# Kernel tuning notes

Measured on AMD Instinct MI355X. Metric: run time of the kernel, lower is better.

The kernel has to match this reference:

```python
import jax, jax.numpy as jnp
import numpy as np

HEADS = 16
KEY_SIZE = 64
SIZE_PER_HEAD = 64
OUT_DIM = HEADS * SIZE_PER_HEAD  # 1024
BIG = 1e10
B, LQ, LK = 2, 2048, 2048


def setup_inputs() -> dict:
    key = jax.random.key(0)
    ks = jax.random.split(key, 8)
    q = jax.random.normal(ks[0], (B, LQ, OUT_DIM), dtype=jnp.float32)
    k = jax.random.normal(ks[1], (B, LK, OUT_DIM), dtype=jnp.float32)
    v = jax.random.normal(ks[2], (B, LK, OUT_DIM), dtype=jnp.float32)
    v_mask = (jax.random.uniform(ks[3], (B, LK)) > 0.1).astype(jnp.float32)
    q_mask = (jax.random.uniform(ks[4], (B, LQ)) > 0.1).astype(jnp.float32)
    # bias-free Linear weights, torch layout [out_features, in_features]
    s = 1.0 / np.sqrt(OUT_DIM)
    Wq = jax.random.normal(ks[5], (HEADS * KEY_SIZE, OUT_DIM), dtype=jnp.float32) * s
    Wk = jax.random.normal(ks[6], (HEADS * KEY_SIZE, OUT_DIM), dtype=jnp.float32) * s
    Wv = jax.random.normal(ks[7], (OUT_DIM, OUT_DIM), dtype=jnp.float32) * s
    return {"q": q, "k": k, "v": v, "v_mask": v_mask, "q_mask": q_mask,
            "Wq": Wq, "Wk": Wk, "Wv": Wv}


def _attention(q, k, v, v_mask, q_mask, Wq, Wk, Wv):
    b, lq, _ = q.shape
    lk = k.shape[1]
    # projections (torch Linear: x @ W.T)
    qw = jnp.einsum('bld,ed->ble', q, Wq).reshape(b, lq, HEADS, KEY_SIZE)
    kw = jnp.einsum('bld,ed->ble', k, Wk).reshape(b, lk, HEADS, KEY_SIZE)
    vw = jnp.einsum('bld,ed->ble', v, Wv).reshape(b, lk, HEADS, SIZE_PER_HEAD)
    # scores [B, H, Lq, Lk]
    a = jnp.einsum('bqhd,bkhd->bhqk', qw, kw) / np.sqrt(KEY_SIZE).astype(np.float32)
    # additive key-padding mask: a - (1 - v_mask) * BIG, broadcast over H and Lq
    a = a - (1.0 - v_mask)[:, None, None, :] * BIG
    # mask_right=True branch: mask = (1 - triu(ones, diag=1)) * BIG, i.e. lower
    # triangle INCLUDING the diagonal is penalized (faithful to source quirk).
    causal = jnp.tril(jnp.ones((lq, lk), dtype=a.dtype)) * BIG  # [Lq, Lk]
    a = a - causal[None, None, :, :]
    a = jax.nn.softmax(a, axis=-1)
    # output [B, Lq, H*dv]
    o = jnp.einsum('bhqk,bkhd->bqhd', a, vw).reshape(b, lq, OUT_DIM)
    o = o * q_mask[:, :, None]
    return o


def reference(q, k, v, v_mask, q_mask, Wq, Wk, Wv):
    return _attention(q, k, v, v_mask, q_mask, Wq, Wk, Wv)
```

## Files before the change

### kernel.cpp

```cpp
#include <hip/hip_runtime.h>
#include <hip/hip_bf16.h>
#include <stdint.h>

#define B_    2
#define SEQ   2048
#define EMB   1024
#define BIGF  1e10f
#define LOG2E 1.4426950408889634f
#define BIG2F (1e10f * LOG2E)
#define C2    (0.125f * LOG2E)

typedef unsigned short u16;
typedef __attribute__((ext_vector_type(4))) u16      u16x4;
typedef __attribute__((ext_vector_type(8))) short    bf8;
typedef __attribute__((ext_vector_type(4))) float    f4;
typedef __attribute__((ext_vector_type(4))) float    fv4;

__device__ inline float bf2f(u16 u){ union{uint32_t i; float f;} v; v.i = ((uint32_t)u) << 16; return v.f; }
__device__ inline u16 f2bf(float f){ union{float f; uint32_t i;} v; v.f = f;
                                     uint32_t r = v.i + 0x7fffu + ((v.i >> 16) & 1u); return (u16)(r >> 16); }
__device__ inline float exp2_hw(float x){ float r; asm("v_exp_f32 %0, %1" : "=v"(r) : "v"(x)); return r; }

__device__ inline void gl_lds16(const void* g, void* l){
  __builtin_amdgcn_global_load_lds((const __attribute__((address_space(1))) uint32_t*)g,
                                   (__attribute__((address_space(3))) uint32_t*)l, 16, 0, 0);
}

struct CvtArgs { const float* src[6]; u16* dst[6]; int n[6]; };

__global__ __launch_bounds__(256) void cvt_bf16(CvtArgs a)
{
  const int seg = blockIdx.y;
  const float* __restrict__ s = a.src[seg];
  u16* __restrict__ d = a.dst[seg];
  const int n = a.n[seg];
  const int i = (blockIdx.x * 256 + threadIdx.x) * 8;
  if (i >= n) return;
  fv4 x0 = *(const fv4*)(s + i);
  fv4 x1 = *(const fv4*)(s + i + 4);
  union { bf8 v; u16 u[8]; } o;
#pragma unroll
  for (int j = 0; j < 4; j++) { o.u[j] = f2bf(x0[j]); o.u[4 + j] = f2bf(x1[j]); }
  *(bf8*)(d + i) = o.v;
}

__global__ __launch_bounds__(256) void proj_gemm(
    const u16* __restrict__ Xq, const u16* __restrict__ Xk, const u16* __restrict__ Xv,
    const u16* __restrict__ Wq, const u16* __restrict__ Wk, const u16* __restrict__ Wv,
    u16* __restrict__ QH, u16* __restrict__ KH, u16* __restrict__ VTB)
{
  __shared__ u16 smem[18432];
  u16* lA = smem;
  u16* lB = smem + 8192;

  const int z = blockIdx.z;
  const u16* X = (z == 0) ? Xq : ((z == 1) ? Xk : Xv);
  const u16* W = (z == 0) ? Wq : ((z == 1) ? Wk : Wv);

  const int tid  = threadIdx.x;
  const int lane = tid & 63;
  const int w    = tid >> 6;
  const int wm   = w >> 1, wn = w & 1;
  const int m0   = blockIdx.x * 128;
  const int n0   = blockIdx.y * 128;
  const int col  = lane & 15, quad = lane >> 4;

  const f4 zero = {0.f, 0.f, 0.f, 0.f};
  f4 acc[4][4];
#pragma unroll
  for (int i = 0; i < 4; i++)
#pragma unroll
    for (int j = 0; j < 4; j++) acc[i][j] = zero;

  for (int k0 = 0; k0 < 1024; k0 += 64) {
    __syncthreads();
#pragma unroll
    for (int j = 0; j < 4; j++) {
      const int kk  = j >> 1;
      const int row = (j & 1) * 64 + w * 16 + (lane >> 2);
      const int cc  = (lane & 3) * 8;
      const size_t g = (size_t)row * 1024 + k0 + kk * 32 + cc;
      gl_lds16(X + (size_t)m0 * 1024 + g, &lA[(j * 256 + w * 64) * 8]);
      gl_lds16(W + (size_t)n0 * 1024 + g, &lB[(j * 256 + w * 64) * 8]);
    }
    __syncthreads();
#pragma unroll
    for (int kk = 0; kk < 2; kk++) {
      const int koff = kk * 4096 + quad * 8;
      bf8 a[4], b[4];
#pragma unroll
      for (int t = 0; t < 4; t++) a[t] = *(const bf8*)&lA[koff + (wm * 64 + t * 16 + col) * 32];
#pragma unroll
      for (int t = 0; t < 4; t++) b[t] = *(const bf8*)&lB[koff + (wn * 64 + t * 16 + col) * 32];
#pragma unroll
      for (int mt = 0; mt < 4; mt++)
#pragma unroll
        for (int nt = 0; nt < 4; nt++)
          acc[mt][nt] = __builtin_amdgcn_mfma_f32_16x16x32_bf16(a[mt], b[nt], acc[mt][nt], 0, 0, 0);
    }
  }

  __syncthreads();
  u16* ep = &smem[w * 4608];

  if (z == 2) {
#pragma unroll
    for (int mt = 0; mt < 4; mt++)
#pragma unroll
      for (int nt = 0; nt < 4; nt++) {
        u16x4 pk = { f2bf(acc[mt][nt][0]), f2bf(acc[mt][nt][1]),
                     f2bf(acc[mt][nt][2]), f2bf(acc[mt][nt][3]) };
        *(u16x4*)&ep[(nt * 16 + col) * 72 + mt * 16 + quad * 4] = pk;
      }
  } else {
#pragma unroll
    for (int mt = 0; mt < 4; mt++)
#pragma unroll
      for (int nt = 0; nt < 4; nt++)
#pragma unroll
        for (int r = 0; r < 4; r++)
          ep[(mt * 16 + quad * 4 + r) * 72 + nt * 16 + col] = f2bf(acc[mt][nt][r]);
  }

  const int bb = m0 >> 11;
  const int h  = (n0 >> 6) + wn;
  const int bh = bb * 16 + h;

  if (z == 0) {
    const int qbase = (m0 & 2047) + wm * 64;
    u16* dst = QH + ((size_t)bh * SEQ + qbase) * 64;
#pragma unroll
    for (int i = 0; i < 8; i++) {
      const int f  = i * 1024 + lane * 16;
      const int ml = i * 8 + (lane >> 3), nl = (lane & 7) * 8;
      *(bf8*)(dst + (f >> 1)) = *(const bf8*)&ep[ml * 72 + nl];
    }
  } else if (z == 1) {
    const int kt = (((m0 & 2047) >> 6) + wm);
    u16* dst = KH + (((size_t)bh * 32 + kt) << 12);
#pragma unroll
    for (int i = 0; i < 8; i++) {
      const int f   = i * 1024 + lane * 16;
      const int dh  = f >> 12;
      const int klc = (f >> 6) & 63;
      const int dlo = (lane & 3) * 8;
      const int fs  = f ^ (((klc >> 1) & 3) << 4);
      *(bf8*)(dst + (fs >> 1)) = *(const bf8*)&ep[klc * 72 + dh * 32 + dlo];
    }
  } else {
    const int kt = (((m0 & 2047) >> 6) + wm);
    u16* dst = VTB + (((size_t)bh * 32 + kt) << 12);
#pragma unroll
    for (int i = 0; i < 8; i++) {
      const int f   = i * 1024 + lane * 16;
      const int kk  = f >> 12;
      const int d   = (f >> 6) & 63;
      const int klo = (lane & 3) * 8;
      const int fs  = f ^ (((d >> 1) & 3) << 4);
      *(bf8*)(dst + (fs >> 1)) = *(const bf8*)&ep[d * 72 + kk * 32 + klo];
    }
  }
}

__global__ __launch_bounds__(256) void sumv(const u16* __restrict__ VTB,
                                            const float* __restrict__ vmask,
                                            float* __restrict__ fb)
{
  const int w = threadIdx.x >> 6, lane = threadIdx.x & 63;
  const int gw = blockIdx.x * 4 + w;
  const int b = gw >> 10, e = gw & 1023;
  const int h = e >> 6, d = e & 63;
  const int bh = b * 16 + h;
  const float* vm = vmask + b * SEQ;
  const int ksw = (lane & 31) ^ (((d >> 1) & 3) << 3);
  float s = 0.f, c = 0.f;
  for (int kt = 0; kt < 32; kt++) {
    const u16 val = VTB[(((size_t)bh * 32 + kt) << 12) + (lane >> 5) * 2048 + d * 32 + ksw];
    const float m = vm[kt * 64 + lane];
    s += m * bf2f(val); c += m;
  }
#pragma unroll
  for (int o = 1; o < 64; o <<= 1) { s += __shfl_xor(s, o); c += __shfl_xor(c, o); }
  if (lane == 0) fb[gw] = s / c;
}

__global__ __launch_bounds__(256) void attn(
    const u16* __restrict__ QH, const u16* __restrict__ KH, const u16* __restrict__ VTB,
    const float* __restrict__ vmask, const float* __restrict__ qmask,
    const float* __restrict__ fb, float* __restrict__ OUT)
{
  __shared__ float pen[SEQ];
  __shared__ u16   sK[2][4096];
  __shared__ u16   sV[2][4096];
  __shared__ u16   P[4 * 16 * 72];

  const int tid = threadIdx.x, lane = tid & 63, w = tid >> 6;
  const int i   = blockIdx.x;
  const int xcd = i & 7;
  const int j   = i >> 3;
  const int qx  = j >> 2;
  const int bh  = xcd + 8 * (j & 3);
  const int b = bh >> 4, h = bh & 15;
  const int col = lane & 15, quad = lane >> 4;
  const int sq8 = (quad ^ ((col >> 1) & 3)) * 8;
  const int wb = w * 16 * 72;

  for (int t = tid; t < SEQ; t += 256)
    pen[t] = (1.0f - vmask[b * SEQ + t]) * BIG2F;

  const u16* kbase = KH  + (((size_t)bh * 32) << 12);
  const u16* vbase = VTB + (((size_t)bh * 32) << 12);

  const int q0 = qx * 64;

  bf8 bQ[2];
#pragma unroll
  for (int dh = 0; dh < 2; dh++)
    bQ[dh] = *(const bf8*)&QH[((size_t)bh * SEQ + q0 + w * 16 + col) * 64 + dh * 32 + quad * 8];

  const f4 zero = {0.f, 0.f, 0.f, 0.f};
  f4 accO[4];
  float l_acc = 0.f;
#pragma unroll
  for (int t = 0; t < 4; t++) accO[t] = zero;

  {
    const size_t toff = ((size_t)qx << 12) + w * 1024 + lane * 8;
    gl_lds16(kbase + toff,       &sK[0][w * 1024]);
    gl_lds16(kbase + toff + 512, &sK[0][w * 1024 + 512]);
    gl_lds16(vbase + toff,       &sV[0][w * 1024]);
    gl_lds16(vbase + toff + 512, &sV[0][w * 1024 + 512]);
  }

  const int ntile = 32 - qx;
  for (int it = 0; it < ntile; it++) {
    __syncthreads();
    if (it + 1 < ntile) {
      const int nb = (it + 1) & 1;
      const size_t toff = ((size_t)(qx + it + 1) << 12) + w * 1024 + lane * 8;
      gl_lds16(kbase + toff,       &sK[nb][w * 1024]);
      gl_lds16(kbase + toff + 512, &sK[nb][w * 1024 + 512]);
      gl_lds16(vbase + toff,       &sV[nb][w * 1024]);
      gl_lds16(vbase + toff + 512, &sV[nb][w * 1024 + 512]);
    }
    const u16* cK = sK[it & 1];
    const u16* cV = sV[it & 1];
    const int k0 = (qx + it) * 64;

    f4 accS[4];
#pragma unroll
    for (int t = 0; t < 4; t++) accS[t] = zero;
    __builtin_amdgcn_s_setprio(1);
#pragma unroll
    for (int nt = 0; nt < 4; nt++)
#pragma unroll
      for (int dh = 0; dh < 2; dh++) {
        bf8 aK = *(const bf8*)&cK[dh * 2048 + (nt * 16 + col) * 32 + sq8];
        accS[nt] = __builtin_amdgcn_mfma_f32_16x16x32_bf16(aK, bQ[dh], accS[nt], 0, 0, 0);
      }
    __builtin_amdgcn_s_setprio(0);

    float p[4][4];
    fv4 pv[4];
#pragma unroll
    for (int nt = 0; nt < 4; nt++) pv[nt] = *(const fv4*)&pen[k0 + nt * 16 + quad * 4];
    if (it == 0) {
#pragma unroll
      for (int nt = 0; nt < 4; nt++)
#pragma unroll
        for (int r = 0; r < 4; r++) {
          float sv = fmaf(accS[nt][r], C2, -pv[nt][r]);
          if (nt * 16 + quad * 4 + r <= w * 16 + col) sv -= BIG2F;
          p[nt][r] = exp2_hw(sv);
        }
    } else {
#pragma unroll
      for (int nt = 0; nt < 4; nt++)
#pragma unroll
        for (int r = 0; r < 4; r++)
          p[nt][r] = exp2_hw(fmaf(accS[nt][r], C2, -pv[nt][r]));
    }
#pragma unroll
    for (int nt = 0; nt < 4; nt++)
      l_acc += (p[nt][0] + p[nt][1]) + (p[nt][2] + p[nt][3]);

#pragma unroll
    for (int nt = 0; nt < 4; nt++) {
      union { u16x4 v; u16 u[4]; } pk;
      union { __hip_bfloat162 h2; u16 u[2]; } c0, c1;
      float2 f01; f01.x = p[nt][0]; f01.y = p[nt][1];
      float2 f23; f23.x = p[nt][2]; f23.y = p[nt][3];
      c0.h2 = __float22bfloat162_rn(f01);
      c1.h2 = __float22bfloat162_rn(f23);
      pk.u[0] = c0.u[0]; pk.u[1] = c0.u[1]; pk.u[2] = c1.u[0]; pk.u[3] = c1.u[1];
      *(u16x4*)&P[wb + col * 72 + nt * 16 + quad * 4] = pk.v;
    }

    __builtin_amdgcn_s_setprio(1);
#pragma unroll
    for (int kk = 0; kk < 2; kk++) {
      bf8 bP = *(const bf8*)&P[wb + col * 72 + kk * 32 + quad * 8];
#pragma unroll
      for (int nt = 0; nt < 4; nt++) {
        bf8 aV = *(const bf8*)&cV[kk * 2048 + (nt * 16 + col) * 32 + sq8];
        accO[nt] = __builtin_amdgcn_mfma_f32_16x16x32_bf16(aV, bP, accO[nt], 0, 0, 0);
      }
    }
    __builtin_amdgcn_s_setprio(0);
  }

  float l = l_acc;
  l += __shfl_xor(l, 16); l += __shfl_xor(l, 32);
  const int q = q0 + w * 16 + col;
  const float qm = qmask[b * SEQ + q];
  float* op = OUT + (size_t)(b * SEQ + q) * EMB + h * 64;
  if (l == 0.0f) {
#pragma unroll
    for (int nt = 0; nt < 4; nt++) {
      fv4 f = *(const fv4*)&fb[b * 1024 + h * 64 + nt * 16 + quad * 4];
      f *= qm;
      *(fv4*)(op + nt * 16 + quad * 4) = f;
    }
  } else {
    const float s = qm / l;
#pragma unroll
    for (int nt = 0; nt < 4; nt++) {
      fv4 f = { accO[nt][0] * s, accO[nt][1] * s, accO[nt][2] * s, accO[nt][3] * s };
      *(fv4*)(op + nt * 16 + quad * 4) = f;
    }
  }
}

extern "C" void kernel_launch(void* const* d_in, const int* in_sizes, int n_in,
                              void* d_out, int out_size, void* d_ws, size_t ws_size,
                              hipStream_t stream)
{
  const float* q  = (const float*)d_in[0];
  const float* k  = (const float*)d_in[1];
  const float* v  = (const float*)d_in[2];
  const float* vm = (const float*)d_in[3];
  const float* qm = (const float*)d_in[4];
  const float* Wq = (const float*)d_in[5];
  const float* Wk = (const float*)d_in[6];
  const float* Wv = (const float*)d_in[7];
  float* out = (float*)d_out;

  const size_t NBIG = (size_t)B_ * SEQ * EMB;
  const size_t NW   = (size_t)EMB * EMB;

  u16* qb  = (u16*)d_ws;
  u16* kb  = qb  + NBIG;
  u16* vb  = kb  + NBIG;
  u16* Wqb = vb  + NBIG;
  u16* Wkb = Wqb + NW;
  u16* Wvb = Wkb + NW;
  u16* QH  = Wvb + NW;
  u16* KH  = QH  + NBIG;
  u16* VTB = KH  + NBIG;
  float* fb = (float*)(VTB + NBIG);

  CvtArgs ca;
  ca.src[0] = q;  ca.dst[0] = qb;  ca.n[0] = (int)NBIG;
  ca.src[1] = k;  ca.dst[1] = kb;  ca.n[1] = (int)NBIG;
  ca.src[2] = v;  ca.dst[2] = vb;  ca.n[2] = (int)NBIG;
  ca.src[3] = Wq; ca.dst[3] = Wqb; ca.n[3] = (int)NW;
  ca.src[4] = Wk; ca.dst[4] = Wkb; ca.n[4] = (int)NW;
  ca.src[5] = Wv; ca.dst[5] = Wvb; ca.n[5] = (int)NW;

  cvt_bf16<<<dim3((unsigned)(NBIG / 8 / 256), 6, 1), 256, 0, stream>>>(ca);
  proj_gemm<<<dim3(32, 8, 3), 256, 0, stream>>>(qb, kb, vb, Wqb, Wkb, Wvb, QH, KH, VTB);
  sumv<<<dim3(512, 1, 1), 256, 0, stream>>>(VTB, vm, fb);
  attn<<<dim3(1024, 1, 1), 256, 0, stream>>>(QH, KH, VTB, vm, qm, fb, out);
}
```

Baseline: 192.0 us.

## Double-buffer projection GEMM LDS tiles and swizzle LDS layout

Restructures the projection GEMM main loop into a double-buffered pipeline with a K-step of 32. The global-to-LDS loads for the next tile are issued before the MFMAs on the current tile, so each iteration needs one barrier instead of two. It also adds an XOR swizzle on the LDS column chunk, applied both when storing and when loading fragments, to reduce LDS bank conflicts. The cost is twice as many loop iterations, each doing less MFMA work per barrier, and it relies on __syncthreads waiting for outstanding global_load_lds operations before the buffer is read.

```diff
diff --git a/kernel.cpp b/kernel.cpp
--- a/kernel.cpp
+++ b/kernel.cpp
@@ -50,9 +50,6 @@
     u16* __restrict__ QH, u16* __restrict__ KH, u16* __restrict__ VTB)
 {
   __shared__ u16 smem[18432];
-  u16* lA = smem;
-  u16* lB = smem + 8192;
-
   const int z = blockIdx.z;
   const u16* X = (z == 0) ? Xq : ((z == 1) ? Xk : Xv);
   const u16* W = (z == 0) ? Wq : ((z == 1) ? Wk : Wv);
@@ -64,6 +61,15 @@
   const int m0   = blockIdx.x * 128;
   const int n0   = blockIdx.y * 128;
   const int col  = lane & 15, quad = lane >> 4;
+  const int sq8  = (quad ^ ((col >> 1) & 3)) * 8;
+
+  const int srow = w * 16 + (lane >> 2);
+  const int sc   = ((lane & 3) ^ ((lane >> 3) & 3)) * 8;
+  const size_t gA0 = (size_t)(m0 + srow) * 1024 + sc;
+  const size_t gA1 = (size_t)(m0 + 64 + srow) * 1024 + sc;
+  const size_t gB0 = (size_t)(n0 + srow) * 1024 + sc;
+  const size_t gB1 = (size_t)(n0 + 64 + srow) * 1024 + sc;
+  const int ldst = w * 512 + lane * 8;
 
   const f4 zero = {0.f, 0.f, 0.f, 0.f};
   f4 acc[4][4];
@@ -72,32 +78,36 @@
 #pragma unroll
     for (int j = 0; j < 4; j++) acc[i][j] = zero;
 
-  for (int k0 = 0; k0 < 1024; k0 += 64) {
+  {
+    gl_lds16(X + gA0, &smem[ldst]);
+    gl_lds16(X + gA1, &smem[2048 + ldst]);
+    gl_lds16(W + gB0, &smem[4096 + ldst]);
+    gl_lds16(W + gB1, &smem[6144 + ldst]);
+  }
+
+#pragma unroll 2
+  for (int t = 0; t < 32; t++) {
     __syncthreads();
-#pragma unroll
-    for (int j = 0; j < 4; j++) {
-      const int kk  = j >> 1;
-      const int row = (j & 1) * 64 + w * 16 + (lane >> 2);
-      const int cc  = (lane & 3) * 8;
-      const size_t g = (size_t)row * 1024 + k0 + kk * 32 + cc;
-      gl_lds16(X + (size_t)m0 * 1024 + g, &lA[(j * 256 + w * 64) * 8]);
-      gl_lds16(W + (size_t)n0 * 1024 + g, &lB[(j * 256 + w * 64) * 8]);
-    }
-    __syncthreads();
-#pragma unroll
-    for (int kk = 0; kk < 2; kk++) {
-      const int koff = kk * 4096 + quad * 8;
-      bf8 a[4], b[4];
-#pragma unroll
-      for (int t = 0; t < 4; t++) a[t] = *(const bf8*)&lA[koff + (wm * 64 + t * 16 + col) * 32];
-#pragma unroll
-      for (int t = 0; t < 4; t++) b[t] = *(const bf8*)&lB[koff + (wn * 64 + t * 16 + col) * 32];
-#pragma unroll
-      for (int mt = 0; mt < 4; mt++)
-#pragma unroll
-        for (int nt = 0; nt < 4; nt++)
-          acc[mt][nt] = __builtin_amdgcn_mfma_f32_16x16x32_bf16(a[mt], b[nt], acc[mt][nt], 0, 0, 0);
-    }
+    if (t + 1 < 32) {
+      const int kn = (t + 1) * 32;
+      u16* nb = smem + ((t + 1) & 1) * 8192;
+      gl_lds16(X + gA0 + kn, &nb[ldst]);
+      gl_lds16(X + gA1 + kn, &nb[2048 + ldst]);
+      gl_lds16(W + gB0 + kn, &nb[4096 + ldst]);
+      gl_lds16(W + gB1 + kn, &nb[6144 + ldst]);
+    }
+    const u16* cA = smem + (t & 1) * 8192;
+    const u16* cB = cA + 4096;
+    bf8 a[4], b[4];
+#pragma unroll
+    for (int tt = 0; tt < 4; tt++) a[tt] = *(const bf8*)&cA[(wm * 64 + tt * 16 + col) * 32 + sq8];
+#pragma unroll
+    for (int tt = 0; tt < 4; tt++) b[tt] = *(const bf8*)&cB[(wn * 64 + tt * 16 + col) * 32 + sq8];
+#pragma unroll
+    for (int mt = 0; mt < 4; mt++)
+#pragma unroll
+      for (int nt = 0; nt < 4; nt++)
+        acc[mt][nt] = __builtin_amdgcn_mfma_f32_16x16x32_bf16(a[mt], b[nt], acc[mt][nt], 0, 0, 0);
   }
 
   __syncthreads();
```

After: 187.7 us. 2.2% less time.
